# Kernel optimization log

Hardware: AMD Instinct MI355X
Metric: run time of the kernel (lower is better)

Reference implementation:

```python
import jax, jax.numpy as jnp
import numpy as np

B, L = 2, 1024
V, D_MODEL, NL = 32, 256, 6
DI, DS, DC, DTR = 512, 16, 4, 16  # d_inner=expand*d_model, d_state, d_conv, dt_rank=d_model/16
NC, MAXL = 10, 2048
ALPHA = 0.1  # observer_alpha


def setup_inputs() -> dict:
    key = jax.random.key(0)
    ks = jax.random.split(key, 16)
    std = 0.02
    emb = std * jax.random.normal(ks[0], (V, D_MODEL), jnp.float32)
    emb = emb.at[0].set(0.0)  # padding_idx=0
    pos_emb = std * jax.random.normal(ks[1], (MAXL, D_MODEL), jnp.float32)
    ln_w = jnp.ones((NL, D_MODEL), jnp.float32)
    ln_b = jnp.zeros((NL, D_MODEL), jnp.float32)
    in_proj_w = std * jax.random.normal(ks[2], (NL, 2 * DI, D_MODEL), jnp.float32)
    conv_w = 0.1 * jax.random.normal(ks[3], (NL, DI, DC), jnp.float32)
    conv_b = jnp.zeros((NL, DI), jnp.float32)
    x_proj_w = std * jax.random.normal(ks[4], (NL, DTR + 2 * DS, DI), jnp.float32)
    dt_proj_w = std * jax.random.normal(ks[5], (NL, DI, DTR), jnp.float32)
    dt_proj_b = jnp.full((NL, DI), -4.6, jnp.float32)  # softplus(-4.6) ~ 0.01 init dt
    A_log = jnp.broadcast_to(jnp.log(jnp.arange(1, DS + 1, dtype=jnp.float32)), (NL, DI, DS)).copy()  # S4D-real
    Dp = jnp.ones((NL, DI), jnp.float32)
    out_proj_w = std * jax.random.normal(ks[6], (NL, D_MODEL, DI), jnp.float32)
    norm_w = jnp.ones((D_MODEL,), jnp.float32)
    norm_b = jnp.zeros((D_MODEL,), jnp.float32)
    cls_w = std * jax.random.normal(ks[7], (NC, D_MODEL), jnp.float32)
    cls_b = jnp.zeros((NC,), jnp.float32)
    x = jax.random.randint(ks[8], (B, L), 0, V, jnp.int64 if jax.config.jax_enable_x64 else jnp.int32)
    mask = jnp.ones((B, L), jnp.int32)
    return dict(emb=emb, pos_emb=pos_emb, ln_w=ln_w, ln_b=ln_b, in_proj_w=in_proj_w,
                conv_w=conv_w, conv_b=conv_b, x_proj_w=x_proj_w, dt_proj_w=dt_proj_w,
                dt_proj_b=dt_proj_b, A_log=A_log, Dp=Dp, out_proj_w=out_proj_w,
                norm_w=norm_w, norm_b=norm_b, cls_w=cls_w, cls_b=cls_b, x=x, mask=mask)


def _ln(x, w, b):
    m = x.mean(-1, keepdims=True)
    v = ((x - m) ** 2).mean(-1, keepdims=True)
    return (x - m) / jnp.sqrt(v + 1e-5) * w + b


def _forward(emb, pos_emb, ln_w, ln_b, in_proj_w, conv_w, conv_b, x_proj_w,
             dt_proj_w, dt_proj_b, A_log, Dp, out_proj_w, norm_w, norm_b,
             cls_w, cls_b, x, mask):
    Bsz, Lsz = x.shape
    h = emb[x] + pos_emb[:Lsz][None, :, :]  # [B,L,D]
    for i in range(NL):
        res = h
        hn = _ln(h, ln_w[i], ln_b[i])
        xz = hn @ in_proj_w[i].T                      # [B,L,2*DI]
        x_in, z = jnp.split(xz, 2, axis=-1)
        # causal depthwise conv1d, kernel DC
        xpad = jnp.pad(x_in, ((0, 0), (DC - 1, 0), (0, 0)))
        xc = conv_b[i]
        for k in range(DC):
            xc = xc + conv_w[i][:, k] * xpad[:, k:k + Lsz, :]
        xc = jax.nn.silu(xc)
        x_dbl = xc @ x_proj_w[i].T                    # [B,L,DTR+2*DS]
        dt = x_dbl[..., :DTR]
        Bm = x_dbl[..., DTR:DTR + DS]
        Cm = x_dbl[..., DTR + DS:]
        delta = jax.nn.softplus(dt @ dt_proj_w[i].T + dt_proj_b[i])  # [B,L,DI]
        A = -jnp.exp(A_log[i])                        # [DI,DS]
        dA = jnp.exp(delta[..., None] * A)            # [B,L,DI,DS]
        dBu = delta[..., None] * Bm[:, :, None, :] * xc[..., None]

        def step(carry, inp):
            hs, hh = carry
            dA_t, dBu_t, c_t = inp
            hs = dA_t * hs + dBu_t                    # true state
            pred = dA_t * hh + dBu_t                  # observer prediction
            hh = pred + ALPHA * (hs - pred)           # Luenberger correction
            y = jnp.einsum('bdn,bn->bd', hh, c_t)
            return (hs, hh), y

        init = (jnp.zeros((Bsz, DI, DS), xc.dtype), jnp.zeros((Bsz, DI, DS), xc.dtype))
        _, ys = jax.lax.scan(step, init,
                             (jnp.moveaxis(dA, 1, 0), jnp.moveaxis(dBu, 1, 0), jnp.moveaxis(Cm, 1, 0)))
        y = jnp.moveaxis(ys, 0, 1) + Dp[i] * xc       # [B,L,DI]
        y = y * jax.nn.silu(z)
        h = y @ out_proj_w[i].T + res
    mf = mask[..., None].astype(h.dtype)
    pooled = (h * mf).sum(axis=1) / mf.sum(axis=1)    # masked mean pool
    pooled = _ln(pooled, norm_w, norm_b)
    return pooled @ cls_w.T + cls_b                   # [B,NC]


def reference(emb, pos_emb, ln_w, ln_b, in_proj_w, conv_w, conv_b, x_proj_w,
              dt_proj_w, dt_proj_b, A_log, Dp, out_proj_w, norm_w, norm_b,
              cls_w, cls_b, x, mask):
    return _forward(emb, pos_emb, ln_w, ln_b, in_proj_w, conv_w, conv_b, x_proj_w,
                    dt_proj_w, dt_proj_b, A_log, Dp, out_proj_w, norm_w, norm_b,
                    cls_w, cls_b, x, mask)
```

## Files before the change

### kernel.cpp

```cpp
#include <hip/hip_runtime.h>
#include <math.h>

#define B_ 2
#define L_ 1024
#define DM 256
#define NL_ 6
#define DI_ 512
#define DS_ 16
#define DC_ 4
#define NC_ 10
#define ALPHA_ 0.1f
#define LC 32
#define NCH (L_/LC)
#define NCHAIN (B_*DI_*DS_)
#define BETA_LC 0.034336838202925124f

typedef unsigned short ushort_t;
typedef __attribute__((ext_vector_type(8))) short s16x8;
typedef __attribute__((ext_vector_type(4))) float f32x4;
typedef __attribute__((ext_vector_type(8))) unsigned short u16x8;

__device__ __forceinline__ float sigmoidf_(float x){ return 1.f/(1.f+__expf(-x)); }
__device__ __forceinline__ ushort_t f2bf(float f){
  union{float f;unsigned u;} c; c.f=f; unsigned u=c.u;
  return (ushort_t)((u + 0x7fffu + ((u>>16)&1u))>>16);
}
__device__ __forceinline__ float bf2f(ushort_t h){
  union{unsigned u;float f;} c; c.u = ((unsigned)h)<<16; return c.f;
}
__device__ __forceinline__ int kidx(int d){ return d + ((d>>7)<<2); }

__global__ void k_embed(const float* __restrict__ emb, const float* __restrict__ pos,
                        const int* __restrict__ ids, float* __restrict__ h){
  int row = blockIdx.x;
  int t = row & (L_-1);
  int d = threadIdx.x;
  int v = ids[row];
  h[(size_t)row*DM + d] = emb[(size_t)v*DM + d] + pos[(size_t)t*DM + d];
}

__global__ void k_cvt2(const float* __restrict__ a, int na, const float* __restrict__ b2,
                       ushort_t* __restrict__ oa, ushort_t* __restrict__ ob, int ntot){
  int i = (blockIdx.x*256 + threadIdx.x)*4;
  if (i >= ntot) return;
  const float* src; ushort_t* dst; int k;
  if (i < na){ src = a; dst = oa; k = i; }
  else       { src = b2; dst = ob; k = i - na; }
  float4 v = *reinterpret_cast<const float4*>(&src[k]);
  ushort4 r;
  r.x = f2bf(v.x); r.y = f2bf(v.y); r.z = f2bf(v.z); r.w = f2bf(v.w);
  *reinterpret_cast<ushort4*>(&dst[k]) = r;
}

__global__ __launch_bounds__(256) void k_gemm_ln(const float* __restrict__ h,
    const ushort_t* __restrict__ W, const float* __restrict__ lw,
    const float* __restrict__ lb, ushort_t* __restrict__ xzb){
  __shared__ ushort_t As[64][264];
  __shared__ ushort_t Ws[64][264];
  int bm = blockIdx.y<<6, bn = blockIdx.x<<6;
  int tid = threadIdx.x;
  {
    int r = tid>>2, q = tid&3;
    const float* src = &h[(size_t)(bm+r)*DM + q*64];
    float4 v[16]; float s1=0.f, s2=0.f;
    #pragma unroll
    for (int i=0;i<16;i++){
      v[i] = *reinterpret_cast<const float4*>(src + i*4);
      s1 += v[i].x+v[i].y+v[i].z+v[i].w;
      s2 += v[i].x*v[i].x+v[i].y*v[i].y+v[i].z*v[i].z+v[i].w*v[i].w;
    }
    s1 += __shfl_xor(s1,1); s2 += __shfl_xor(s2,1);
    s1 += __shfl_xor(s1,2); s2 += __shfl_xor(s2,2);
    float mean = s1*(1.f/DM);
    float rstd = rsqrtf(s2*(1.f/DM) - mean*mean + 1e-5f);
    #pragma unroll
    for (int i=0;i<16;i++){
      int c = q*64 + i*4;
      ushort4 o;
      o.x = f2bf((v[i].x-mean)*rstd*lw[c+0]+lb[c+0]);
      o.y = f2bf((v[i].y-mean)*rstd*lw[c+1]+lb[c+1]);
      o.z = f2bf((v[i].z-mean)*rstd*lw[c+2]+lb[c+2]);
      o.w = f2bf((v[i].w-mean)*rstd*lw[c+3]+lb[c+3]);
      *reinterpret_cast<ushort4*>(&As[r][c]) = o;
    }
    const ushort_t* ws = &W[(size_t)(bn+r)*DM + q*64];
    #pragma unroll
    for (int i=0;i<8;i++)
      *reinterpret_cast<u16x8*>(&Ws[r][q*64+i*8]) = *reinterpret_cast<const u16x8*>(ws + i*8);
  }
  __syncthreads();
  int lane = tid&63, wid = tid>>6;
  int wm = (wid>>1)<<5, wn = (wid&1)<<5;
  int fr = lane&15, fk = (lane>>4)<<3;
  f32x4 acc[2][2] = {};
  #pragma unroll
  for (int k0=0;k0<DM;k0+=32){
    s16x8 a0 = *reinterpret_cast<const s16x8*>(&As[wm+fr][k0+fk]);
    s16x8 a1 = *reinterpret_cast<const s16x8*>(&As[wm+16+fr][k0+fk]);
    s16x8 b0 = *reinterpret_cast<const s16x8*>(&Ws[wn+fr][k0+fk]);
    s16x8 b1 = *reinterpret_cast<const s16x8*>(&Ws[wn+16+fr][k0+fk]);
    acc[0][0] = __builtin_amdgcn_mfma_f32_16x16x32_bf16(a0,b0,acc[0][0],0,0,0);
    acc[0][1] = __builtin_amdgcn_mfma_f32_16x16x32_bf16(a0,b1,acc[0][1],0,0,0);
    acc[1][0] = __builtin_amdgcn_mfma_f32_16x16x32_bf16(a1,b0,acc[1][0],0,0,0);
    acc[1][1] = __builtin_amdgcn_mfma_f32_16x16x32_bf16(a1,b1,acc[1][1],0,0,0);
  }
  int cr = (lane>>4)<<2, cc = lane&15;
  #pragma unroll
  for (int i=0;i<2;i++)
    #pragma unroll
    for (int j=0;j<2;j++){
      int row = bm + wm + (i<<4) + cr;
      int col = bn + wn + (j<<4) + cc;
      #pragma unroll
      for (int r=0;r<4;r++)
        xzb[(size_t)(row+r)*(2*DI_) + col] = f2bf(acc[i][j][r]);
    }
}

__global__ __launch_bounds__(256) void k_xpc(const ushort_t* __restrict__ xzb,
    const float* __restrict__ cw, const float* __restrict__ cb,
    const float* __restrict__ xw, ushort_t* __restrict__ xcb,
    float* __restrict__ xdbl){
  __shared__ float sxz[7][DI_];
  __shared__ float sx[4][DI_+16];
  int tid = threadIdx.x;
  int m0 = blockIdx.x*4;
  #pragma unroll
  for (int q=0;q<2;q++){
    int idx = q*256 + tid;
    if (idx < 448){
      int i = idx>>6, c8 = (idx&63)<<3;
      int mr = m0 - 3 + i;
      if (mr >= 0){
        u16x8 v = *reinterpret_cast<const u16x8*>(&xzb[(size_t)mr*(2*DI_) + c8]);
        #pragma unroll
        for (int e=0;e<8;e++) sxz[i][c8+e] = bf2f((ushort_t)v[e]);
      } else {
        #pragma unroll
        for (int e=0;e<8;e++) sxz[i][c8+e] = 0.f;
      }
    }
  }
  __syncthreads();
  {
    int r = tid>>6, c8 = (tid&63)<<3;
    int t = (m0 + r) & (L_-1);
    u16x8 outv;
    #pragma unroll
    for (int e=0;e<8;e++){
      int d = c8 + e;
      float acc = cb[d];
      #pragma unroll
      for (int k=0;k<4;k++)
        if (t-3+k >= 0) acc = fmaf(cw[d*4+k], sxz[r+k][d], acc);
      float sv = acc * sigmoidf_(acc);
      sx[r][kidx(d)] = sv;
      outv[e] = (short)f2bf(sv);
    }
    *reinterpret_cast<u16x8*>(&xcb[(size_t)(m0+r)*DI_ + c8]) = outv;
  }
  __syncthreads();
  if (tid < 192){
    int o = tid>>2, q = tid&3;
    const float* wp = &xw[(size_t)o*DI_ + q*128];
    const int qb = q*132;
    float a0=0.f,a1=0.f,a2=0.f,a3=0.f;
    #pragma unroll 8
    for (int k4=0;k4<32;k4++){
      float4 wv = *reinterpret_cast<const float4*>(wp + k4*4);
      int kk = qb + k4*4;
      float4 x0 = *reinterpret_cast<const float4*>(&sx[0][kk]);
      float4 x1 = *reinterpret_cast<const float4*>(&sx[1][kk]);
      float4 x2 = *reinterpret_cast<const float4*>(&sx[2][kk]);
      float4 x3 = *reinterpret_cast<const float4*>(&sx[3][kk]);
      a0 = fmaf(x0.x,wv.x,a0); a0 = fmaf(x0.y,wv.y,a0); a0 = fmaf(x0.z,wv.z,a0); a0 = fmaf(x0.w,wv.w,a0);
      a1 = fmaf(x1.x,wv.x,a1); a1 = fmaf(x1.y,wv.y,a1); a1 = fmaf(x1.z,wv.z,a1); a1 = fmaf(x1.w,wv.w,a1);
      a2 = fmaf(x2.x,wv.x,a2); a2 = fmaf(x2.y,wv.y,a2); a2 = fmaf(x2.z,wv.z,a2); a2 = fmaf(x2.w,wv.w,a2);
      a3 = fmaf(x3.x,wv.x,a3); a3 = fmaf(x3.y,wv.y,a3); a3 = fmaf(x3.z,wv.z,a3); a3 = fmaf(x3.w,wv.w,a3);
    }
    a0 += __shfl_xor(a0,1); a0 += __shfl_xor(a0,2);
    a1 += __shfl_xor(a1,1); a1 += __shfl_xor(a1,2);
    a2 += __shfl_xor(a2,1); a2 += __shfl_xor(a2,2);
    a3 += __shfl_xor(a3,1); a3 += __shfl_xor(a3,2);
    if (q==0){
      xdbl[(size_t)(m0+0)*48+o]=a0;
      xdbl[(size_t)(m0+1)*48+o]=a1;
      xdbl[(size_t)(m0+2)*48+o]=a2;
      xdbl[(size_t)(m0+3)*48+o]=a3;
    }
  }
}

__global__ __launch_bounds__(256) void k_scanA(const ushort_t* __restrict__ xcb,
    const float* __restrict__ xdbl, const float* __restrict__ dtw,
    const float* __restrict__ dtb, const float* __restrict__ A_log,
    float4* __restrict__ smry){
  int j = blockIdx.x, g = blockIdx.y, b = blockIdx.z;
  int tid = threadIdx.x;
  int n = tid&15, dg = tid>>4;
  int d0 = g*16;
  int mbase = b*L_ + j*LC;
  __shared__ float sbd[LC][48];
  __shared__ float sdtw[16][16];
  __shared__ float sxv[LC][16];
  __shared__ float sdel[LC][16];
  {
    const float4* xsrc = reinterpret_cast<const float4*>(xdbl + (size_t)mbase*48);
    reinterpret_cast<float4*>(&sbd[0][0])[tid] = xsrc[tid];
    if (tid < 128) reinterpret_cast<float4*>(&sbd[0][0])[256+tid] = xsrc[256+tid];
    if (tid < 64){
      int row = tid>>1, half = tid&1;
      u16x8 v = *reinterpret_cast<const u16x8*>(&xcb[(size_t)(mbase+row)*DI_ + d0 + half*8]);
      #pragma unroll
      for (int e=0;e<8;e++) sxv[row][half*8+e] = bf2f((ushort_t)v[e]);
    } else if (tid < 128){
      int s = tid-64, row = s>>2, c4 = (s&3)<<2;
      *reinterpret_cast<float4*>(&sdtw[row][c4]) =
        *reinterpret_cast<const float4*>(&dtw[(size_t)(d0+row)*16 + c4]);
    }
  }
  __syncthreads();
  #pragma unroll
  for (int q=0;q<2;q++){
    int p = q*256 + tid;
    int t = p>>4, dd = p&15;
    float acc = dtb[d0+dd];
    #pragma unroll
    for (int k=0;k<16;k++) acc = fmaf(sbd[t][k], sdtw[dd][k], acc);
    sdel[t][dd] = (acc>20.f)? acc : log1pf(__expf(acc));
  }
  __syncthreads();
  float a = -__expf(A_log[(d0+dg)*DS_ + n]);
  float hs=0.f, hh=0.f, cp=1.f;
  #pragma unroll
  for (int tt=0; tt<LC; tt+=8){
    float dA8[8], dBu8[8];
    #pragma unroll
    for (int t=0;t<8;t++){
      float dv = sdel[tt+t][dg];
      dA8[t]  = __expf(dv*a);
      dBu8[t] = dv * sxv[tt+t][dg] * sbd[tt+t][16+n];
    }
    #pragma unroll
    for (int t=0;t<8;t++){
      float mix = fmaf(ALPHA_, hs-hh, hh);
      hs = fmaf(dA8[t], hs, dBu8[t]);
      hh = fmaf(dA8[t], mix, dBu8[t]);
      cp *= dA8[t];
    }
  }
  smry[(size_t)j*NCHAIN + (size_t)(b*DI_+d0)*DS_ + tid] = float4{cp,hs,hh,0.f};
}

__global__ __launch_bounds__(256) void k_scanB(const float4* __restrict__ smry,
    float2* __restrict__ initArr){
  int g = blockIdx.x, b = blockIdx.y;
  int c = (b*DI_ + g*16)*DS_ + threadIdx.x;
  float hs=0.f, hh=0.f;
  #pragma unroll
  for (int j=0;j<NCH;j++){
    size_t o = (size_t)j*NCHAIN + c;
    float4 v = smry[o];
    initArr[o] = float2{hs,hh};
    float snew = fmaf(v.x, hs, v.y);
    hh = fmaf(v.x, fmaf(BETA_LC, hh-hs, hs), v.z);
    hs = snew;
  }
}

__global__ __launch_bounds__(256) void k_scanC(const ushort_t* __restrict__ xcb,
    const float* __restrict__ xdbl, const ushort_t* __restrict__ xzb,
    const float* __restrict__ dtw, const float* __restrict__ dtb,
    const float* __restrict__ A_log, const float* __restrict__ Dp,
    const float2* __restrict__ initArr, ushort_t* __restrict__ y2b){
  int j = blockIdx.x, g = blockIdx.y, b = blockIdx.z;
  int tid = threadIdx.x;
  int n = tid&15, dg = tid>>4;
  int d0 = g*16;
  int mbase = b*L_ + j*LC;
  int chain = (b*DI_+d0)*DS_ + tid;
  float2 iv = initArr[(size_t)j*NCHAIN + chain];
  __shared__ float sbd[LC][48];
  __shared__ float sdtw[16][16];
  __shared__ float sxv[LC][16];
  __shared__ float sdel[LC][16];
  __shared__ float sz[LC][16];
  __shared__ float sy[LC][16];
  {
    const float4* xsrc = reinterpret_cast<const float4*>(xdbl + (size_t)mbase*48);
    reinterpret_cast<float4*>(&sbd[0][0])[tid] = xsrc[tid];
    if (tid < 128) reinterpret_cast<float4*>(&sbd[0][0])[256+tid] = xsrc[256+tid];
    if (tid < 64){
      int row = tid>>1, half = tid&1;
      u16x8 v = *reinterpret_cast<const u16x8*>(&xcb[(size_t)(mbase+row)*DI_ + d0 + half*8]);
      #pragma unroll
      for (int e=0;e<8;e++) sxv[row][half*8+e] = bf2f((ushort_t)v[e]);
    } else if (tid < 128){
      int s = tid-64, row = s>>1, half = s&1;
      u16x8 v = *reinterpret_cast<const u16x8*>(&xzb[(size_t)(mbase+row)*(2*DI_) + DI_ + d0 + half*8]);
      #pragma unroll
      for (int e=0;e<8;e++) sz[row][half*8+e] = bf2f((ushort_t)v[e]);
    } else if (tid < 192){
      int s = tid-128, row = s>>2, c4 = (s&3)<<2;
      *reinterpret_cast<float4*>(&sdtw[row][c4]) =
        *reinterpret_cast<const float4*>(&dtw[(size_t)(d0+row)*16 + c4]);
    }
  }
  __syncthreads();
  #pragma unroll
  for (int q=0;q<2;q++){
    int p = q*256 + tid;
    int t = p>>4, dd = p&15;
    float acc = dtb[d0+dd];
    #pragma unroll
    for (int k=0;k<16;k++) acc = fmaf(sbd[t][k], sdtw[dd][k], acc);
    sdel[t][dd] = (acc>20.f)? acc : log1pf(__expf(acc));
  }
  __syncthreads();
  float a = -__expf(A_log[(d0+dg)*DS_ + n]);
  float hs = iv.x, hh = iv.y;
  #pragma unroll
  for (int tt=0; tt<LC; tt+=8){
    float dA8[8], dBu8[8], yv8[8];
    #pragma unroll
    for (int t=0;t<8;t++){
      float dv = sdel[tt+t][dg];
      dA8[t]  = __expf(dv*a);
      dBu8[t] = dv * sxv[tt+t][dg] * sbd[tt+t][16+n];
    }
    #pragma unroll
    for (int t=0;t<8;t++){
      float mix = fmaf(ALPHA_, hs-hh, hh);
      hs = fmaf(dA8[t], hs, dBu8[t]);
      hh = fmaf(dA8[t], mix, dBu8[t]);
      yv8[t] = hh * sbd[tt+t][32+n];
    }
    #pragma unroll
    for (int t=0;t<8;t++){
      yv8[t] += __shfl_xor(yv8[t],1,16);
      yv8[t] += __shfl_xor(yv8[t],2,16);
      yv8[t] += __shfl_xor(yv8[t],4,16);
      yv8[t] += __shfl_xor(yv8[t],8,16);
    }
    if (n==0){
      #pragma unroll
      for (int t=0;t<8;t++) sy[tt+t][dg] = yv8[t];
    }
  }
  __syncthreads();
  float dpv = Dp[d0 + (tid&15)];
  #pragma unroll
  for (int idx=0; idx<2; ++idx){
    int flat = idx*256 + tid;
    int t2 = flat>>4, dd = flat&15;
    float xvv = sxv[t2][dd];
    float zv  = sz [t2][dd];
    float yfin = (sy[t2][dd] + dpv*xvv) * (zv*sigmoidf_(zv));
    y2b[(size_t)(mbase + t2)*DI_ + d0 + dd] = f2bf(yfin);
  }
}

__global__ __launch_bounds__(256) void k_gemm_out(const ushort_t* __restrict__ A,
    const ushort_t* __restrict__ W, float* __restrict__ h){
  __shared__ ushort_t As[32][264];
  __shared__ ushort_t Ws[64][264];
  int bm = blockIdx.y<<5, bn = blockIdx.x<<6;
  int tid = threadIdx.x;
  int lane = tid&63, wid = tid>>6;
  int wm = (wid>>1)<<4, wn = (wid&1)<<5;
  int fr = lane&15, fk = (lane>>4)<<3;
  f32x4 acc[2] = {};
  for (int k0=0;k0<DI_;k0+=256){
    {
      int r = tid>>3, q = tid&7;
      const ushort_t* src = &A[(size_t)(bm+r)*DI_ + k0 + q*32];
      #pragma unroll
      for (int i=0;i<4;i++)
        *reinterpret_cast<u16x8*>(&As[r][q*32+i*8]) = *reinterpret_cast<const u16x8*>(src+i*8);
      int r2 = tid>>2, q2 = tid&3;
      const ushort_t* ws = &W[(size_t)(bn+r2)*DI_ + k0 + q2*64];
      #pragma unroll
      for (int i=0;i<8;i++)
        *reinterpret_cast<u16x8*>(&Ws[r2][q2*64+i*8]) = *reinterpret_cast<const u16x8*>(ws+i*8);
    }
    __syncthreads();
    #pragma unroll
    for (int k=0;k<256;k+=32){
      s16x8 a0 = *reinterpret_cast<const s16x8*>(&As[wm+fr][k+fk]);
      s16x8 b0 = *reinterpret_cast<const s16x8*>(&Ws[wn+fr][k+fk]);
      s16x8 b1 = *reinterpret_cast<const s16x8*>(&Ws[wn+16+fr][k+fk]);
      acc[0] = __builtin_amdgcn_mfma_f32_16x16x32_bf16(a0,b0,acc[0],0,0,0);
      acc[1] = __builtin_amdgcn_mfma_f32_16x16x32_bf16(a0,b1,acc[1],0,0,0);
    }
    __syncthreads();
  }
  int cr = (lane>>4)<<2, cc = lane&15;
  #pragma unroll
  for (int jj=0;jj<2;jj++){
    int row = bm + wm + cr;
    int col = bn + wn + (jj<<4) + cc;
    #pragma unroll
    for (int r=0;r<4;r++){
      size_t idx2 = (size_t)(row+r)*DM + col;
      h[idx2] += acc[jj][r];
    }
  }
}

__global__ __launch_bounds__(256) void k_pool(const float* __restrict__ h,
    const int* __restrict__ mask, float* __restrict__ partial){
  int p = blockIdx.x, b = blockIdx.y, d = threadIdx.x;
  int t0 = p*64;
  __shared__ float sm[64];
  if (d < 64) sm[d] = (float)mask[b*L_ + t0 + d];
  __syncthreads();
  const float* hp = &h[(size_t)(b*L_ + t0)*DM + d];
  float s = 0.f;
  #pragma unroll 8
  for (int i=0;i<64;i++)
    s = fmaf(sm[i], hp[(size_t)i*DM], s);
  partial[(size_t)(b*16+p)*DM + d] = s;
}

__global__ __launch_bounds__(256) void k_head(const float* __restrict__ partial,
    const int* __restrict__ mask, const float* __restrict__ nw, const float* __restrict__ nb,
    const float* __restrict__ cw, const float* __restrict__ cb, float* __restrict__ out){
  int b = blockIdx.x, d = threadIdx.x;
  int4 mi = *reinterpret_cast<const int4*>(&mask[b*L_ + d*4]);
  float cnt = (float)(mi.x + mi.y + mi.z + mi.w);
  #pragma unroll
  for (int o=32;o>0;o>>=1) cnt += __shfl_down(cnt,o);
  __shared__ float ac[4];
  __shared__ float scnt;
  int wid = d>>6, lane = d&63;
  if (lane==0) ac[wid] = cnt;
  __syncthreads();
  if (d==0) scnt = ac[0]+ac[1]+ac[2]+ac[3];
  __syncthreads();
  float s = 0.f;
  #pragma unroll
  for (int p=0;p<16;p++) s += partial[(size_t)(b*16+p)*DM + d];
  float v = s / scnt;
  float s1 = v, s2 = v*v;
  #pragma unroll
  for (int o=32;o>0;o>>=1){ s1 += __shfl_down(s1,o); s2 += __shfl_down(s2,o); }
  __shared__ float a1[4], a2[4];
  __shared__ float mv[2];
  if (lane==0){ a1[wid]=s1; a2[wid]=s2; }
  __syncthreads();
  if (d==0){
    float t1=a1[0]+a1[1]+a1[2]+a1[3];
    float t2=a2[0]+a2[1]+a2[2]+a2[3];
    float m = t1/(float)DM;
    mv[0]=m; mv[1]=rsqrtf(t2/(float)DM - m*m + 1e-5f);
  }
  __syncthreads();
  __shared__ float sp[DM];
  sp[d] = (v-mv[0])*mv[1]*nw[d]+nb[d];
  __syncthreads();
  __shared__ float cpart[NC_][16];
  if (d < NC_*16){
    int c = d>>4, q = d&15;
    float acc = 0.f;
    #pragma unroll
    for (int k=0;k<16;k++) acc = fmaf(sp[q*16+k], cw[(size_t)c*DM+q*16+k], acc);
    cpart[c][q] = acc;
  }
  __syncthreads();
  if (d < NC_){
    float acc = cb[d];
    #pragma unroll
    for (int q=0;q<16;q++) acc += cpart[d][q];
    out[b*NC_+d] = acc;
  }
}

extern "C" void kernel_launch(void* const* d_in, const int* in_sizes, int n_in,
                              void* d_out, int out_size, void* d_ws, size_t ws_size,
                              hipStream_t stream){
  const float* emb   = (const float*)d_in[0];
  const float* pos   = (const float*)d_in[1];
  const float* ln_w  = (const float*)d_in[2];
  const float* ln_b  = (const float*)d_in[3];
  const float* ipw   = (const float*)d_in[4];
  const float* cw    = (const float*)d_in[5];
  const float* cb    = (const float*)d_in[6];
  const float* xpw   = (const float*)d_in[7];
  const float* dtw   = (const float*)d_in[8];
  const float* dtb   = (const float*)d_in[9];
  const float* A_log = (const float*)d_in[10];
  const float* Dp    = (const float*)d_in[11];
  const float* opw   = (const float*)d_in[12];
  const float* nw    = (const float*)d_in[13];
  const float* nb    = (const float*)d_in[14];
  const float* clw   = (const float*)d_in[15];
  const float* clb   = (const float*)d_in[16];
  const int*   ids   = (const int*)d_in[17];
  const int*   mask  = (const int*)d_in[18];
  float* out = (float*)d_out;

  float* ws    = (float*)d_ws;
  float* h     = ws;
  float* xdbl  = h + 524288;
  float* part  = xdbl + 98304;
  float4* smry = (float4*)(part + 8192);
  float2* initA= (float2*)((float*)smry + 2097152);
  ushort_t* xzb  = (ushort_t*)((float*)initA + 1048576);
  ushort_t* xcb  = xzb + 2097152;
  ushort_t* y2b  = xcb + 1048576;
  ushort_t* ipwb = y2b + 1048576;
  ushort_t* opwb = ipwb + 1572864;

  const int NA = 6*2*DI_*DM, NB = 6*DM*DI_;
  k_cvt2<<<dim3((NA+NB)/1024), 256, 0, stream>>>(ipw, NA, opw, ipwb, opwb, NA+NB);
  k_embed<<<dim3(B_*L_), dim3(DM), 0, stream>>>(emb, pos, ids, h);

  for (int l=0; l<NL_; ++l){
    k_gemm_ln<<<dim3(16, 32), 256, 0, stream>>>(
        h, ipwb + (size_t)l*2*DI_*DM, ln_w + l*DM, ln_b + l*DM, xzb);
    k_xpc<<<dim3((B_*L_)/4), 256, 0, stream>>>(
        xzb, cw + l*DI_*DC_, cb + l*DI_, xpw + (size_t)l*48*DI_, xcb, xdbl);
    k_scanA<<<dim3(NCH, DI_/16, B_), 256, 0, stream>>>(
        xcb, xdbl, dtw + (size_t)l*DI_*16, dtb + l*DI_,
        A_log + (size_t)l*DI_*DS_, smry);
    k_scanB<<<dim3(DI_/16, B_), 256, 0, stream>>>(smry, initA);
    k_scanC<<<dim3(NCH, DI_/16, B_), 256, 0, stream>>>(
        xcb, xdbl, xzb, dtw + (size_t)l*DI_*16, dtb + l*DI_,
        A_log + (size_t)l*DI_*DS_, Dp + l*DI_, initA, y2b);
    k_gemm_out<<<dim3(DM/64, (B_*L_)/32), 256, 0, stream>>>(
        y2b, opwb + (size_t)l*DM*DI_, h);
  }
  k_pool<<<dim3(16, B_), 256, 0, stream>>>(h, mask, part);
  k_head<<<dim3(B_), 256, 0, stream>>>(part, mask, nw, nb, clw, clb, out);
}
```

Before: 484.6 us.

## Fuse LN+in_proj GEMM, conv, x_proj, dt_proj and chunk scan summary into one kernel

```diff
diff --git a/kernel.cpp b/kernel.cpp
--- a/kernel.cpp
+++ b/kernel.cpp
@@ -28,7 +28,6 @@
 __device__ __forceinline__ float bf2f(ushort_t h){
   union{unsigned u;float f;} c; c.u = ((unsigned)h)<<16; return c.f;
 }
-__device__ __forceinline__ int kidx(int d){ return d + ((d>>7)<<2); }
 
 __global__ void k_embed(const float* __restrict__ emb, const float* __restrict__ pos,
                         const int* __restrict__ ids, float* __restrict__ h){
@@ -39,217 +38,274 @@
   h[(size_t)row*DM + d] = emb[(size_t)v*DM + d] + pos[(size_t)t*DM + d];
 }
 
-__global__ void k_cvt2(const float* __restrict__ a, int na, const float* __restrict__ b2,
-                       ushort_t* __restrict__ oa, ushort_t* __restrict__ ob, int ntot){
-  int i = (blockIdx.x*256 + threadIdx.x)*4;
-  if (i >= ntot) return;
-  const float* src; ushort_t* dst; int k;
-  if (i < na){ src = a; dst = oa; k = i; }
-  else       { src = b2; dst = ob; k = i - na; }
+__global__ void k_cvt4(const float* __restrict__ a, const float* __restrict__ b2,
+                       const float* __restrict__ c3, const float* __restrict__ d4,
+                       ushort_t* __restrict__ oa, ushort_t* __restrict__ ob,
+                       ushort_t* __restrict__ oc, ushort_t* __restrict__ od,
+                       int na, int nb, int nc2, int nd){
+  int k = (blockIdx.x*256 + threadIdx.x)*4;
+  const float* src; ushort_t* dst;
+  if (k < na){ src=a; dst=oa; }
+  else { k -= na;
+    if (k < nb){ src=b2; dst=ob; }
+    else { k -= nb;
+      if (k < nc2){ src=c3; dst=oc; }
+      else { k -= nc2;
+        if (k >= nd) return;
+        src=d4; dst=od; } } }
   float4 v = *reinterpret_cast<const float4*>(&src[k]);
   ushort4 r;
   r.x = f2bf(v.x); r.y = f2bf(v.y); r.z = f2bf(v.z); r.w = f2bf(v.w);
   *reinterpret_cast<ushort4*>(&dst[k]) = r;
 }
 
-__global__ __launch_bounds__(256) void k_gemm_ln(const float* __restrict__ h,
-    const ushort_t* __restrict__ W, const float* __restrict__ lw,
-    const float* __restrict__ lb, ushort_t* __restrict__ xzb){
-  __shared__ ushort_t As[64][264];
-  __shared__ ushort_t Ws[64][264];
-  int bm = blockIdx.y<<6, bn = blockIdx.x<<6;
+#define OFF_HN   0
+#define OFF_WS   25344
+#define OFF_SXB  92928
+#define OFF_SXC  0
+#define OFF_SXW  33280
+#define OFF_SDT  83200
+#define OFF_SBB  85248
+#define OFF_SDEL 92928
+#define OFF_SDTW 126208
+#define SMEM_SZ  142848
+
+__global__ __launch_bounds__(512) void k_fusedA(
+    const float* __restrict__ h, const ushort_t* __restrict__ Wip,
+    const float* __restrict__ lw, const float* __restrict__ lb,
+    const float* __restrict__ cw, const float* __restrict__ cb,
+    const ushort_t* __restrict__ xpwb, const ushort_t* __restrict__ dtwb,
+    const float* __restrict__ dtb, const float* __restrict__ A_log,
+    ushort_t* __restrict__ xcb, ushort_t* __restrict__ szb,
+    float* __restrict__ xdbl, float4* __restrict__ smry)
+{
+  __shared__ __align__(16) char smem[SMEM_SZ];
+  ushort_t* HN  = (ushort_t*)(smem + OFF_HN);
+  ushort_t* WS  = (ushort_t*)(smem + OFF_WS);
+  ushort_t* SXB = (ushort_t*)(smem + OFF_SXB);
+  ushort_t* SXC = (ushort_t*)(smem + OFF_SXC);
+  ushort_t* SXW = (ushort_t*)(smem + OFF_SXW);
+  float*    SDT = (float*)(smem + OFF_SDT);
+  float*    SBB = (float*)(smem + OFF_SBB);
+  ushort_t* SDEL= (ushort_t*)(smem + OFF_SDEL);
+  ushort_t* SDTW= (ushort_t*)(smem + OFF_SDTW);
+
+  int j = blockIdx.x, b = blockIdx.y;
+  int m0 = b*L_ + j*LC;
   int tid = threadIdx.x;
+  int lane = tid & 63, wv = tid >> 6;
+
+  if (tid < 384){
+    int r = tid >> 3, s = tid & 7;
+    if (j == 0 && r < 16){
+      ushort4 z4; z4.x=z4.y=z4.z=z4.w=0;
+      #pragma unroll
+      for (int i=0;i<8;i++)
+        *reinterpret_cast<ushort4*>(&HN[r*264 + s*32 + i*4]) = z4;
+    } else {
+      int gr = m0 - 16 + r;
+      const float* src = &h[(size_t)gr*DM + s*32];
+      float4 v[8]; float s1=0.f, s2=0.f;
+      #pragma unroll
+      for (int i=0;i<8;i++){
+        v[i] = *reinterpret_cast<const float4*>(src + i*4);
+        s1 += v[i].x+v[i].y+v[i].z+v[i].w;
+        s2 += v[i].x*v[i].x+v[i].y*v[i].y+v[i].z*v[i].z+v[i].w*v[i].w;
+      }
+      s1 += __shfl_xor(s1,1); s2 += __shfl_xor(s2,1);
+      s1 += __shfl_xor(s1,2); s2 += __shfl_xor(s2,2);
+      s1 += __shfl_xor(s1,4); s2 += __shfl_xor(s2,4);
+      float mean = s1*(1.f/DM);
+      float rstd = rsqrtf(s2*(1.f/DM) - mean*mean + 1e-5f);
+      #pragma unroll
+      for (int i=0;i<8;i++){
+        int c = s*32 + i*4;
+        ushort4 o;
+        o.x = f2bf((v[i].x-mean)*rstd*lw[c+0]+lb[c+0]);
+        o.y = f2bf((v[i].y-mean)*rstd*lw[c+1]+lb[c+1]);
+        o.z = f2bf((v[i].z-mean)*rstd*lw[c+2]+lb[c+2]);
+        o.w = f2bf((v[i].w-mean)*rstd*lw[c+3]+lb[c+3]);
+        *reinterpret_cast<ushort4*>(&HN[r*264 + c]) = o;
+      }
+    }
+  }
+  __syncthreads();
+
+  int fr = lane & 15, fk = (lane>>4)<<3;
+  int cr = (lane>>4)<<2, cc = lane & 15;
+  for (int nt=0; nt<8; ++nt){
+    {
+      int r = tid >> 2, q = tid & 3;
+      const ushort_t* src = &Wip[(size_t)(nt*128 + r)*DM + q*64];
+      #pragma unroll
+      for (int i=0;i<8;i++)
+        *reinterpret_cast<u16x8*>(&WS[r*264 + q*64 + i*8]) =
+          *reinterpret_cast<const u16x8*>(src + i*8);
+    }
+    __syncthreads();
+    if (nt < 4){
+      #pragma unroll
+      for (int i=0;i<3;i++){
+        int u = wv*3 + i; int s_c = u & 7, s_r = u >> 3;
+        f32x4 acc = {};
+        #pragma unroll
+        for (int ks=0; ks<8; ++ks){
+          s16x8 af = *reinterpret_cast<const s16x8*>(&HN[(s_r*16+fr)*264 + ks*32 + fk]);
+          s16x8 bf = *reinterpret_cast<const s16x8*>(&WS[(s_c*16+fr)*264 + ks*32 + fk]);
+          acc = __builtin_amdgcn_mfma_f32_16x16x32_bf16(af, bf, acc, 0,0,0);
+        }
+        #pragma unroll
+        for (int rg=0; rg<4; ++rg)
+          SXB[(s_r*16 + cr + rg)*520 + nt*128 + s_c*16 + cc] = f2bf(acc[rg]);
+      }
+    } else {
+      #pragma unroll
+      for (int i=0;i<2;i++){
+        int u = wv*2 + i; int s_c = u & 7, s_r = u >> 3;
+        f32x4 acc = {};
+        #pragma unroll
+        for (int ks=0; ks<8; ++ks){
+          s16x8 af = *reinterpret_cast<const s16x8*>(&HN[(16 + s_r*16+fr)*264 + ks*32 + fk]);
+          s16x8 bf = *reinterpret_cast<const s16x8*>(&WS[(s_c*16+fr)*264 + ks*32 + fk]);
+          acc = __builtin_amdgcn_mfma_f32_16x16x32_bf16(af, bf, acc, 0,0,0);
+        }
+        #pragma unroll
+        for (int rg=0; rg<4; ++rg){
+          float v = acc[rg];
+          float sv = v * sigmoidf_(v);
+          szb[(size_t)(m0 + s_r*16 + cr + rg)*DI_ + (nt-4)*128 + s_c*16 + cc] = f2bf(sv);
+        }
+      }
+    }
+    __syncthreads();
+  }
+
   {
-    int r = tid>>2, q = tid&3;
-    const float* src = &h[(size_t)(bm+r)*DM + q*64];
-    float4 v[16]; float s1=0.f, s2=0.f;
-    #pragma unroll
-    for (int i=0;i<16;i++){
-      v[i] = *reinterpret_cast<const float4*>(src + i*4);
-      s1 += v[i].x+v[i].y+v[i].z+v[i].w;
-      s2 += v[i].x*v[i].x+v[i].y*v[i].y+v[i].z*v[i].z+v[i].w*v[i].w;
-    }
-    s1 += __shfl_xor(s1,1); s2 += __shfl_xor(s2,1);
-    s1 += __shfl_xor(s1,2); s2 += __shfl_xor(s2,2);
-    float mean = s1*(1.f/DM);
-    float rstd = rsqrtf(s2*(1.f/DM) - mean*mean + 1e-5f);
-    #pragma unroll
-    for (int i=0;i<16;i++){
-      int c = q*64 + i*4;
-      ushort4 o;
-      o.x = f2bf((v[i].x-mean)*rstd*lw[c+0]+lb[c+0]);
-      o.y = f2bf((v[i].y-mean)*rstd*lw[c+1]+lb[c+1]);
-      o.z = f2bf((v[i].z-mean)*rstd*lw[c+2]+lb[c+2]);
-      o.w = f2bf((v[i].w-mean)*rstd*lw[c+3]+lb[c+3]);
-      *reinterpret_cast<ushort4*>(&As[r][c]) = o;
-    }
-    const ushort_t* ws = &W[(size_t)(bn+r)*DM + q*64];
-    #pragma unroll
-    for (int i=0;i<8;i++)
-      *reinterpret_cast<u16x8*>(&Ws[r][q*64+i*8]) = *reinterpret_cast<const u16x8*>(ws + i*8);
-  }
-  __syncthreads();
-  int lane = tid&63, wid = tid>>6;
-  int wm = (wid>>1)<<5, wn = (wid&1)<<5;
-  int fr = lane&15, fk = (lane>>4)<<3;
-  f32x4 acc[2][2] = {};
-  #pragma unroll
-  for (int k0=0;k0<DM;k0+=32){
-    s16x8 a0 = *reinterpret_cast<const s16x8*>(&As[wm+fr][k0+fk]);
-    s16x8 a1 = *reinterpret_cast<const s16x8*>(&As[wm+16+fr][k0+fk]);
-    s16x8 b0 = *reinterpret_cast<const s16x8*>(&Ws[wn+fr][k0+fk]);
-    s16x8 b1 = *reinterpret_cast<const s16x8*>(&Ws[wn+16+fr][k0+fk]);
-    acc[0][0] = __builtin_amdgcn_mfma_f32_16x16x32_bf16(a0,b0,acc[0][0],0,0,0);
-    acc[0][1] = __builtin_amdgcn_mfma_f32_16x16x32_bf16(a0,b1,acc[0][1],0,0,0);
-    acc[1][0] = __builtin_amdgcn_mfma_f32_16x16x32_bf16(a1,b0,acc[1][0],0,0,0);
-    acc[1][1] = __builtin_amdgcn_mfma_f32_16x16x32_bf16(a1,b1,acc[1][1],0,0,0);
-  }
-  int cr = (lane>>4)<<2, cc = lane&15;
-  #pragma unroll
-  for (int i=0;i<2;i++)
-    #pragma unroll
-    for (int j=0;j<2;j++){
-      int row = bm + wm + (i<<4) + cr;
-      int col = bn + wn + (j<<4) + cc;
-      #pragma unroll
-      for (int r=0;r<4;r++)
-        xzb[(size_t)(row+r)*(2*DI_) + col] = f2bf(acc[i][j][r]);
-    }
-}
-
-__global__ __launch_bounds__(256) void k_xpc(const ushort_t* __restrict__ xzb,
-    const float* __restrict__ cw, const float* __restrict__ cb,
-    const float* __restrict__ xw, ushort_t* __restrict__ xcb,
-    float* __restrict__ xdbl){
-  __shared__ float sxz[7][DI_];
-  __shared__ float sx[4][DI_+16];
-  int tid = threadIdx.x;
-  int m0 = blockIdx.x*4;
-  #pragma unroll
-  for (int q=0;q<2;q++){
-    int idx = q*256 + tid;
-    if (idx < 448){
-      int i = idx>>6, c8 = (idx&63)<<3;
-      int mr = m0 - 3 + i;
-      if (mr >= 0){
-        u16x8 v = *reinterpret_cast<const u16x8*>(&xzb[(size_t)mr*(2*DI_) + c8]);
+    int c8 = (tid & 63) * 8;
+    int r4 = (tid >> 6) * 4;
+    float cwv[8][4]; float cbv[8];
+    #pragma unroll
+    for (int e=0;e<8;e++){
+      float4 w4 = *reinterpret_cast<const float4*>(&cw[(c8+e)*4]);
+      cwv[e][0]=w4.x; cwv[e][1]=w4.y; cwv[e][2]=w4.z; cwv[e][3]=w4.w;
+      cbv[e] = cb[c8+e];
+    }
+    #pragma unroll
+    for (int rr=0; rr<4; ++rr){
+      int t2 = r4 + rr;
+      u16x8 ov;
+      #pragma unroll
+      for (int e=0;e<8;e++){
+        float acc = cbv[e];
         #pragma unroll
-        for (int e=0;e<8;e++) sxz[i][c8+e] = bf2f((ushort_t)v[e]);
-      } else {
-        #pragma unroll
-        for (int e=0;e<8;e++) sxz[i][c8+e] = 0.f;
-      }
-    }
-  }
-  __syncthreads();
+        for (int k=0;k<4;k++)
+          acc = fmaf(cwv[e][k], bf2f(SXB[(13 + t2 + k)*520 + c8 + e]), acc);
+        float sv = acc * sigmoidf_(acc);
+        ov[e] = (short)f2bf(sv);
+      }
+      *reinterpret_cast<u16x8*>(&SXC[t2*520 + c8]) = ov;
+      *reinterpret_cast<u16x8*>(&xcb[(size_t)(m0+t2)*DI_ + c8]) = ov;
+    }
+  }
+  __syncthreads();
+
   {
-    int r = tid>>6, c8 = (tid&63)<<3;
-    int t = (m0 + r) & (L_-1);
-    u16x8 outv;
-    #pragma unroll
-    for (int e=0;e<8;e++){
-      int d = c8 + e;
-      float acc = cb[d];
-      #pragma unroll
-      for (int k=0;k<4;k++)
-        if (t-3+k >= 0) acc = fmaf(cw[d*4+k], sxz[r+k][d], acc);
-      float sv = acc * sigmoidf_(acc);
-      sx[r][kidx(d)] = sv;
-      outv[e] = (short)f2bf(sv);
-    }
-    *reinterpret_cast<u16x8*>(&xcb[(size_t)(m0+r)*DI_ + c8]) = outv;
-  }
-  __syncthreads();
-  if (tid < 192){
-    int o = tid>>2, q = tid&3;
-    const float* wp = &xw[(size_t)o*DI_ + q*128];
-    const int qb = q*132;
-    float a0=0.f,a1=0.f,a2=0.f,a3=0.f;
-    #pragma unroll 8
-    for (int k4=0;k4<32;k4++){
-      float4 wv = *reinterpret_cast<const float4*>(wp + k4*4);
-      int kk = qb + k4*4;
-      float4 x0 = *reinterpret_cast<const float4*>(&sx[0][kk]);
-      float4 x1 = *reinterpret_cast<const float4*>(&sx[1][kk]);
-      float4 x2 = *reinterpret_cast<const float4*>(&sx[2][kk]);
-      float4 x3 = *reinterpret_cast<const float4*>(&sx[3][kk]);
-      a0 = fmaf(x0.x,wv.x,a0); a0 = fmaf(x0.y,wv.y,a0); a0 = fmaf(x0.z,wv.z,a0); a0 = fmaf(x0.w,wv.w,a0);
-      a1 = fmaf(x1.x,wv.x,a1); a1 = fmaf(x1.y,wv.y,a1); a1 = fmaf(x1.z,wv.z,a1); a1 = fmaf(x1.w,wv.w,a1);
-      a2 = fmaf(x2.x,wv.x,a2); a2 = fmaf(x2.y,wv.y,a2); a2 = fmaf(x2.z,wv.z,a2); a2 = fmaf(x2.w,wv.w,a2);
-      a3 = fmaf(x3.x,wv.x,a3); a3 = fmaf(x3.y,wv.y,a3); a3 = fmaf(x3.z,wv.z,a3); a3 = fmaf(x3.w,wv.w,a3);
-    }
-    a0 += __shfl_xor(a0,1); a0 += __shfl_xor(a0,2);
-    a1 += __shfl_xor(a1,1); a1 += __shfl_xor(a1,2);
-    a2 += __shfl_xor(a2,1); a2 += __shfl_xor(a2,2);
-    a3 += __shfl_xor(a3,1); a3 += __shfl_xor(a3,2);
-    if (q==0){
-      xdbl[(size_t)(m0+0)*48+o]=a0;
-      xdbl[(size_t)(m0+1)*48+o]=a1;
-      xdbl[(size_t)(m0+2)*48+o]=a2;
-      xdbl[(size_t)(m0+3)*48+o]=a3;
-    }
-  }
-}
-
-__global__ __launch_bounds__(256) void k_scanA(const ushort_t* __restrict__ xcb,
-    const float* __restrict__ xdbl, const float* __restrict__ dtw,
-    const float* __restrict__ dtb, const float* __restrict__ A_log,
-    float4* __restrict__ smry){
-  int j = blockIdx.x, g = blockIdx.y, b = blockIdx.z;
-  int tid = threadIdx.x;
-  int n = tid&15, dg = tid>>4;
-  int d0 = g*16;
-  int mbase = b*L_ + j*LC;
-  __shared__ float sbd[LC][48];
-  __shared__ float sdtw[16][16];
-  __shared__ float sxv[LC][16];
-  __shared__ float sdel[LC][16];
+    #pragma unroll
+    for (int i=0;i<6;i++){
+      int t4 = i*512 + tid;
+      int o = t4 >> 6, k8 = (t4 & 63) * 8;
+      *reinterpret_cast<u16x8*>(&SXW[o*520 + k8]) =
+        *reinterpret_cast<const u16x8*>(&xpwb[(size_t)o*DI_ + k8]);
+    }
+    int d = tid;
+    *reinterpret_cast<u16x8*>(&SDTW[d*16])   = *reinterpret_cast<const u16x8*>(&dtwb[d*16]);
+    *reinterpret_cast<u16x8*>(&SDTW[d*16+8]) = *reinterpret_cast<const u16x8*>(&dtwb[d*16+8]);
+  }
+  __syncthreads();
+
   {
-    const float4* xsrc = reinterpret_cast<const float4*>(xdbl + (size_t)mbase*48);
-    reinterpret_cast<float4*>(&sbd[0][0])[tid] = xsrc[tid];
-    if (tid < 128) reinterpret_cast<float4*>(&sbd[0][0])[256+tid] = xsrc[256+tid];
-    if (tid < 64){
-      int row = tid>>1, half = tid&1;
-      u16x8 v = *reinterpret_cast<const u16x8*>(&xcb[(size_t)(mbase+row)*DI_ + d0 + half*8]);
-      #pragma unroll
-      for (int e=0;e<8;e++) sxv[row][half*8+e] = bf2f((ushort_t)v[e]);
-    } else if (tid < 128){
-      int s = tid-64, row = s>>2, c4 = (s&3)<<2;
-      *reinterpret_cast<float4*>(&sdtw[row][c4]) =
-        *reinterpret_cast<const float4*>(&dtw[(size_t)(d0+row)*16 + c4]);
-    }
-  }
-  __syncthreads();
-  #pragma unroll
-  for (int q=0;q<2;q++){
-    int p = q*256 + tid;
-    int t = p>>4, dd = p&15;
-    float acc = dtb[d0+dd];
-    #pragma unroll
-    for (int k=0;k<16;k++) acc = fmaf(sbd[t][k], sdtw[dd][k], acc);
-    sdel[t][dd] = (acc>20.f)? acc : log1pf(__expf(acc));
-  }
-  __syncthreads();
-  float a = -__expf(A_log[(d0+dg)*DS_ + n]);
-  float hs=0.f, hh=0.f, cp=1.f;
-  #pragma unroll
-  for (int tt=0; tt<LC; tt+=8){
-    float dA8[8], dBu8[8];
-    #pragma unroll
-    for (int t=0;t<8;t++){
-      float dv = sdel[tt+t][dg];
-      dA8[t]  = __expf(dv*a);
-      dBu8[t] = dv * sxv[tt+t][dg] * sbd[tt+t][16+n];
-    }
-    #pragma unroll
-    for (int t=0;t<8;t++){
-      float mix = fmaf(ALPHA_, hs-hh, hh);
-      hs = fmaf(dA8[t], hs, dBu8[t]);
-      hh = fmaf(dA8[t], mix, dBu8[t]);
-      cp *= dA8[t];
-    }
-  }
-  smry[(size_t)j*NCHAIN + (size_t)(b*DI_+d0)*DS_ + tid] = float4{cp,hs,hh,0.f};
+    int r = tid >> 4, p = tid & 15;
+    float a0=0.f, a1=0.f, a2=0.f;
+    const ushort_t* xr = &SXC[r*520];
+    #pragma unroll 4
+    for (int k8=0; k8<512; k8+=8){
+      u16x8 xv = *reinterpret_cast<const u16x8*>(&xr[k8]);
+      u16x8 w0 = *reinterpret_cast<const u16x8*>(&SXW[p*520 + k8]);
+      u16x8 w1 = *reinterpret_cast<const u16x8*>(&SXW[(p+16)*520 + k8]);
+      u16x8 w2 = *reinterpret_cast<const u16x8*>(&SXW[(p+32)*520 + k8]);
+      #pragma unroll
+      for (int e=0;e<8;e++){
+        float xf = bf2f((ushort_t)xv[e]);
+        a0 = fmaf(xf, bf2f((ushort_t)w0[e]), a0);
+        a1 = fmaf(xf, bf2f((ushort_t)w1[e]), a1);
+        a2 = fmaf(xf, bf2f((ushort_t)w2[e]), a2);
+      }
+    }
+    SDT[r*16+p] = a0;
+    SBB[r*16+p] = a1;
+    size_t xb = (size_t)(m0 + r)*48;
+    xdbl[xb + p]      = a0;
+    xdbl[xb + 16 + p] = a1;
+    xdbl[xb + 32 + p] = a2;
+  }
+  __syncthreads();
+
+  {
+    int d = tid;
+    u16x8 wa = *reinterpret_cast<const u16x8*>(&SDTW[d*16]);
+    u16x8 wb = *reinterpret_cast<const u16x8*>(&SDTW[d*16+8]);
+    float wk[16];
+    #pragma unroll
+    for (int e=0;e<8;e++){ wk[e] = bf2f((ushort_t)wa[e]); wk[8+e] = bf2f((ushort_t)wb[e]); }
+    float bias = dtb[d];
+    #pragma unroll
+    for (int t=0;t<LC;t++){
+      const float* sd = &SDT[t*16];
+      float acc = bias;
+      #pragma unroll
+      for (int k=0;k<16;k++) acc = fmaf(sd[k], wk[k], acc);
+      float sp = (acc>20.f)? acc : log1pf(__expf(acc));
+      SDEL[t*520 + d] = f2bf(sp);
+    }
+  }
+  __syncthreads();
+
+  {
+    int d = tid;
+    float a[16];
+    #pragma unroll
+    for (int q=0;q<4;q++){
+      float4 v = *reinterpret_cast<const float4*>(&A_log[d*DS_ + q*4]);
+      a[q*4+0] = -__expf(v.x); a[q*4+1] = -__expf(v.y);
+      a[q*4+2] = -__expf(v.z); a[q*4+3] = -__expf(v.w);
+    }
+    float hs[16], hh[16];
+    #pragma unroll
+    for (int n=0;n<16;n++){ hs[n]=0.f; hh[n]=0.f; }
+    float sumdv = 0.f;
+    #pragma unroll 4
+    for (int t=0;t<LC;t++){
+      float dv = bf2f(SDEL[t*520 + d]);
+      float xv = bf2f(SXC[t*520 + d]);
+      float cmn = dv * xv;
+      sumdv += dv;
+      const float* sb = &SBB[t*16];
+      #pragma unroll
+      for (int n=0;n<16;n++){
+        float dA = __expf(dv * a[n]);
+        float dBu = cmn * sb[n];
+        float mix = fmaf(ALPHA_, hs[n]-hh[n], hh[n]);
+        hs[n] = fmaf(dA, hs[n], dBu);
+        hh[n] = fmaf(dA, mix, dBu);
+      }
+    }
+    size_t base = (size_t)j*NCHAIN + (size_t)(b*DI_ + d)*DS_;
+    #pragma unroll
+    for (int n=0;n<16;n++){
+      float cp = __expf(a[n]*sumdv);
+      smry[base + n] = float4{cp, hs[n], hh[n], 0.f};
+    }
+  }
 }
 
 __global__ __launch_bounds__(256) void k_scanB(const float4* __restrict__ smry,
@@ -269,7 +325,7 @@
 }
 
 __global__ __launch_bounds__(256) void k_scanC(const ushort_t* __restrict__ xcb,
-    const float* __restrict__ xdbl, const ushort_t* __restrict__ xzb,
+    const float* __restrict__ xdbl, const ushort_t* __restrict__ szb,
     const float* __restrict__ dtw, const float* __restrict__ dtb,
     const float* __restrict__ A_log, const float* __restrict__ Dp,
     const float2* __restrict__ initArr, ushort_t* __restrict__ y2b){
@@ -297,7 +353,7 @@
       for (int e=0;e<8;e++) sxv[row][half*8+e] = bf2f((ushort_t)v[e]);
     } else if (tid < 128){
       int s = tid-64, row = s>>1, half = s&1;
-      u16x8 v = *reinterpret_cast<const u16x8*>(&xzb[(size_t)(mbase+row)*(2*DI_) + DI_ + d0 + half*8]);
+      u16x8 v = *reinterpret_cast<const u16x8*>(&szb[(size_t)(mbase+row)*DI_ + d0 + half*8]);
       #pragma unroll
       for (int e=0;e<8;e++) sz[row][half*8+e] = bf2f((ushort_t)v[e]);
     } else if (tid < 192){
@@ -354,8 +410,8 @@
     int flat = idx*256 + tid;
     int t2 = flat>>4, dd = flat&15;
     float xvv = sxv[t2][dd];
-    float zv  = sz [t2][dd];
-    float yfin = (sy[t2][dd] + dpv*xvv) * (zv*sigmoidf_(zv));
+    float szv = sz [t2][dd];
+    float yfin = (sy[t2][dd] + dpv*xvv) * szv;
     y2b[(size_t)(mbase + t2)*DI_ + d0 + dd] = f2bf(yfin);
   }
 }
@@ -505,27 +561,29 @@
   float* part  = xdbl + 98304;
   float4* smry = (float4*)(part + 8192);
   float2* initA= (float2*)((float*)smry + 2097152);
-  ushort_t* xzb  = (ushort_t*)((float*)initA + 1048576);
-  ushort_t* xcb  = xzb + 2097152;
-  ushort_t* y2b  = xcb + 1048576;
+  ushort_t* xcb  = (ushort_t*)((float*)initA + 1048576);
+  ushort_t* szb  = xcb + 1048576;
+  ushort_t* y2b  = szb + 1048576;
   ushort_t* ipwb = y2b + 1048576;
   ushort_t* opwb = ipwb + 1572864;
-
-  const int NA = 6*2*DI_*DM, NB = 6*DM*DI_;
-  k_cvt2<<<dim3((NA+NB)/1024), 256, 0, stream>>>(ipw, NA, opw, ipwb, opwb, NA+NB);
+  ushort_t* xpwb = opwb + 786432;
+  ushort_t* dtwb = xpwb + 147456;
+
+  const int NA = 6*2*DI_*DM, NB = 6*DM*DI_, NX = 6*48*DI_, ND = 6*DI_*16;
+  k_cvt4<<<dim3(((NA+NB+NX+ND)/4 + 255)/256), 256, 0, stream>>>(
+      ipw, opw, xpw, dtw, ipwb, opwb, xpwb, dtwb, NA, NB, NX, ND);
   k_embed<<<dim3(B_*L_), dim3(DM), 0, stream>>>(emb, pos, ids, h);
 
   for (int l=0; l<NL_; ++l){
-    k_gemm_ln<<<dim3(16, 32), 256, 0, stream>>>(
-        h, ipwb + (size_t)l*2*DI_*DM, ln_w + l*DM, ln_b + l*DM, xzb);
-    k_xpc<<<dim3((B_*L_)/4), 256, 0, stream>>>(
-        xzb, cw + l*DI_*DC_, cb + l*DI_, xpw + (size_t)l*48*DI_, xcb, xdbl);
-    k_scanA<<<dim3(NCH, DI_/16, B_), 256, 0, stream>>>(
-        xcb, xdbl, dtw + (size_t)l*DI_*16, dtb + l*DI_,
-        A_log + (size_t)l*DI_*DS_, smry);
+    k_fusedA<<<dim3(NCH, B_), 512, 0, stream>>>(
+        h, ipwb + (size_t)l*2*DI_*DM, ln_w + l*DM, ln_b + l*DM,
+        cw + l*DI_*DC_, cb + l*DI_,
+        xpwb + (size_t)l*48*DI_, dtwb + (size_t)l*DI_*16,
+        dtb + l*DI_, A_log + (size_t)l*DI_*DS_,
+        xcb, szb, xdbl, smry);
     k_scanB<<<dim3(DI_/16, B_), 256, 0, stream>>>(smry, initA);
     k_scanC<<<dim3(NCH, DI_/16, B_), 256, 0, stream>>>(
-        xcb, xdbl, xzb, dtw + (size_t)l*DI_*16, dtb + l*DI_,
+        xcb, xdbl, szb, dtw + (size_t)l*DI_*16, dtb + l*DI_,
         A_log + (size_t)l*DI_*DS_, Dp + l*DI_, initA, y2b);
     k_gemm_out<<<dim3(DM/64, (B_*L_)/32), 256, 0, stream>>>(
         y2b, opwb + (size_t)l*DM*DI_, h);
```

Measured after the change: 717.0 us. 48.0% more time.
